# Performance work log

Hardware: AMD Instinct MI355X
Metric: run time of the kernel (lower is better)

## Reference

```python
import jax, jax.numpy as jnp
import numpy as np

NUM_EXPERTS = 64
HIDDEN = 2048
SINKHORN_ITERS = 30
EPS = 1e-08


def setup_inputs() -> dict:
    key = jax.random.key(0)
    k1, k2 = jax.random.split(key)
    hidden_states = jax.random.normal(k1, (4, 2048, HIDDEN), dtype=jnp.float32)
    # torch Linear default init ~ U(-1/sqrt(H), 1/sqrt(H))
    bound = 1.0 / np.sqrt(HIDDEN)
    W = jax.random.uniform(k2, (NUM_EXPERTS, HIDDEN), dtype=jnp.float32,
                           minval=-bound, maxval=bound)
    return {"hidden_states": hidden_states, "W": W}


def _sinkhorn(cost, num_iters=SINKHORN_ITERS):
    # cost: (T, E) float32 logits
    cost = jnp.exp(cost)
    T, E = cost.shape
    d0 = jnp.ones((T,), dtype=cost.dtype)
    d1 = jnp.ones((E,), dtype=cost.dtype)

    def body(i, carry):
        d0, d1 = carry
        d0 = (1.0 / T) / (jnp.sum(d1 * cost, axis=1) + EPS)
        d1 = (1.0 / E) / (jnp.sum(d0[:, None] * cost, axis=0) + EPS)
        return (d0, d1)

    d0, d1 = jax.lax.fori_loop(0, num_iters, body, (d0, d1))
    return d1 * cost * d0[:, None]


def reference(hidden_states, W):
    # router logits: (B, S, H) @ (H, E) -> flatten to (T, E)
    logits = jnp.einsum('bsh,eh->bse', hidden_states, W)
    router_logits = logits.reshape(-1, NUM_EXPERTS)
    # expert affinities (original uses float64 sigmoid; use float32 for jax default)
    expert_affinities = jax.nn.sigmoid(router_logits.astype(jnp.float32))
    expert_affinities = expert_affinities.astype(hidden_states.dtype)
    # Sinkhorn balancing on detached logits (training path)
    sinkroute = _sinkhorn(jax.lax.stop_gradient(router_logits).astype(jnp.float32))
    expert_index = jnp.argmax(sinkroute, axis=1, keepdims=True).astype(jnp.int32)
    return (router_logits, expert_affinities, expert_index)
```

## Files before the change

### kernel.cpp

```cpp
#include <hip/hip_runtime.h>
#include <math.h>

#define T_TOKENS 8192
#define NEXP 64
#define HID 2048
#define NITER 30
#define SINK_BLOCKS 32
#define NCHUNK 32
#define QPC 512
#define WREG 131072

typedef __bf16 bf16_t;
typedef bf16_t bf16x8 __attribute__((ext_vector_type(8)));
typedef bf16_t bf16x4 __attribute__((ext_vector_type(4)));
typedef float  f32x4  __attribute__((ext_vector_type(4)));

__device__ __forceinline__ void gload_lds16(const void* g, void* l) {
    __builtin_amdgcn_global_load_lds(
        (const __attribute__((address_space(1))) unsigned int*)g,
        (__attribute__((address_space(3))) unsigned int*)l, 16, 0, 0);
}

__global__ __launch_bounds__(256)
void prep_whl(const float* __restrict__ W, bf16_t* __restrict__ wsw)
{
    int gid = blockIdx.x * 256 + threadIdx.x;
    int region = gid >> 14;
    int qid = gid & 16383;
    int c = qid >> 9, L = qid & 511;
    int r = L >> 3, slot = L & 7;
    int qi = slot ^ (r & 7);
    const float* src = W + (size_t)r * HID + c * 64 + qi * 8;
    float4 v0 = *(const float4*)src;
    float4 v1 = *(const float4*)(src + 4);
    float x[8] = {v0.x, v0.y, v0.z, v0.w, v1.x, v1.y, v1.z, v1.w};
    bf16x8 q;
#pragma unroll
    for (int i = 0; i < 8; i++) {
        bf16_t h = (bf16_t)x[i];
        q[i] = (region == 0) ? h : (bf16_t)(x[i] - (float)h);
    }
    *(bf16x8*)(wsw + (size_t)region * WREG + (size_t)qid * 8) = q;
}

__global__ __launch_bounds__(256, 2)
void gemm_mfma_split(const float* __restrict__ A, const bf16_t* __restrict__ Wq,
                     float* __restrict__ out)
{
    __shared__ bf16_t sA[2][2][16 * 64];
    __shared__ bf16_t sW[2][2][64 * 64];
    __shared__ float  red[2 * 512];

    const int tid = threadIdx.x, lane = tid & 63, wv = tid >> 6;
    const int tok0 = blockIdx.x * 16;
    const int s = wv >> 1, nh = wv & 1;
    const int g = lane >> 4, m = lane & 15;

    f32x4 acc0 = {0.f, 0.f, 0.f, 0.f}, acc1 = {0.f, 0.f, 0.f, 0.f};

    const int ar = tid >> 4, ak4 = tid & 15;
    const int a_woff = ar * 64 + (((ak4 >> 1) ^ (ar & 7)) << 3) + ((ak4 & 1) << 2);
    const float* ag = A + (size_t)(tok0 + ar) * HID + ak4 * 4;

    const bf16_t* whg = Wq;
    const bf16_t* wlg = Wq + WREG;

    const int aq = s * 4 + g;
    const int a_roff  = m * 64 + ((aq ^ (m & 7)) << 3);
    const int n0 = nh * 32 + m, n1 = n0 + 16;
    const int b_roff0 = n0 * 64 + ((aq ^ (n0 & 7)) << 3);
    const int b_roff1 = n1 * 64 + ((aq ^ (n1 & 7)) << 3);

    {
        float4 av = *(const float4*)ag;
        float xs[4] = {av.x, av.y, av.z, av.w};
        bf16x4 hq, lq;
#pragma unroll
        for (int i = 0; i < 4; i++) {
            bf16_t h = (bf16_t)xs[i];
            hq[i] = h; lq[i] = (bf16_t)(xs[i] - (float)h);
        }
        *(bf16x4*)&sA[0][0][a_woff] = hq;
        *(bf16x4*)&sA[0][1][a_woff] = lq;
#pragma unroll
        for (int j = 0; j < 2; j++) {
            size_t q = (size_t)(j * 256 + wv * 64 + lane) * 8;
            gload_lds16(whg + q, &sW[0][0][(j * 256 + wv * 64) * 8]);
            gload_lds16(wlg + q, &sW[0][1][(j * 256 + wv * 64) * 8]);
        }
    }
    __syncthreads();

    for (int c = 0; c < NCHUNK; ++c) {
        const int buf = c & 1, nb = buf ^ 1;
        if (c + 1 < NCHUNK) {
            const int cn = c + 1;
            float4 av = *(const float4*)(ag + cn * 64);
#pragma unroll
            for (int j = 0; j < 2; j++) {
                size_t q = (size_t)(cn * QPC + j * 256 + wv * 64 + lane) * 8;
                gload_lds16(whg + q, &sW[nb][0][(j * 256 + wv * 64) * 8]);
                gload_lds16(wlg + q, &sW[nb][1][(j * 256 + wv * 64) * 8]);
            }
            float xs[4] = {av.x, av.y, av.z, av.w};
            bf16x4 hq, lq;
#pragma unroll
            for (int i = 0; i < 4; i++) {
                bf16_t h = (bf16_t)xs[i];
                hq[i] = h; lq[i] = (bf16_t)(xs[i] - (float)h);
            }
            *(bf16x4*)&sA[nb][0][a_woff] = hq;
            *(bf16x4*)&sA[nb][1][a_woff] = lq;
        }

        bf16x8 fAh  = *(const bf16x8*)&sA[buf][0][a_roff];
        bf16x8 fAl  = *(const bf16x8*)&sA[buf][1][a_roff];
        bf16x8 fWh0 = *(const bf16x8*)&sW[buf][0][b_roff0];
        bf16x8 fWl0 = *(const bf16x8*)&sW[buf][1][b_roff0];
        bf16x8 fWh1 = *(const bf16x8*)&sW[buf][0][b_roff1];
        bf16x8 fWl1 = *(const bf16x8*)&sW[buf][1][b_roff1];

        acc0 = __builtin_amdgcn_mfma_f32_16x16x32_bf16(fAh, fWh0, acc0, 0, 0, 0);
        acc0 = __builtin_amdgcn_mfma_f32_16x16x32_bf16(fAh, fWl0, acc0, 0, 0, 0);
        acc0 = __builtin_amdgcn_mfma_f32_16x16x32_bf16(fAl, fWh0, acc0, 0, 0, 0);
        acc1 = __builtin_amdgcn_mfma_f32_16x16x32_bf16(fAh, fWh1, acc1, 0, 0, 0);
        acc1 = __builtin_amdgcn_mfma_f32_16x16x32_bf16(fAh, fWl1, acc1, 0, 0, 0);
        acc1 = __builtin_amdgcn_mfma_f32_16x16x32_bf16(fAl, fWh1, acc1, 0, 0, 0);
        __syncthreads();
    }

    if (s == 1) {
#pragma unroll
        for (int i = 0; i < 4; i++) {
            red[nh * 512 + lane * 8 + i]     = acc0[i];
            red[nh * 512 + lane * 8 + 4 + i] = acc1[i];
        }
    }
    __syncthreads();
    if (s == 0) {
        const int t0 = tok0 + (lane >> 4) * 4;
#pragma unroll
        for (int i = 0; i < 4; i++) {
            float v0 = acc0[i] + red[nh * 512 + lane * 8 + i];
            float v1 = acc1[i] + red[nh * 512 + lane * 8 + 4 + i];
            int t = t0 + i;
            out[(size_t)t * 64 + n0] = v0;
            out[(size_t)t * 64 + n1] = v1;
            float s0 = (v0 >= 0.f) ? 1.f / (1.f + expf(-v0))
                                   : expf(v0) / (1.f + expf(v0));
            float s1 = (v1 >= 0.f) ? 1.f / (1.f + expf(-v1))
                                   : expf(v1) / (1.f + expf(v1));
            out[(size_t)T_TOKENS * 64 + (size_t)t * 64 + n0] = s0;
            out[(size_t)T_TOKENS * 64 + (size_t)t * 64 + n1] = s1;
        }
    }
}

__global__ __launch_bounds__(256, 1)
void sinkhorn_v3(const float* __restrict__ logits,
                 float* __restrict__ out_idx,
                 float* __restrict__ part)
{
    __shared__ float tile[4][64 * 68];
    __shared__ float d1_lds[64];
    __shared__ float pl[4][64];
    const int tid = threadIdx.x;
    const int bid = blockIdx.x;
    const int wave = tid >> 6, lane = tid & 63;
    const int t = bid * 256 + tid;

    float c[64];
#pragma unroll
    for (int e4 = 0; e4 < 16; e4++) {
        float4 v = *(const float4*)(logits + (size_t)t * 64 + e4 * 4);
        c[e4 * 4 + 0] = expf(v.x);
        c[e4 * 4 + 1] = expf(v.y);
        c[e4 * 4 + 2] = expf(v.z);
        c[e4 * 4 + 3] = expf(v.w);
    }
    if (tid < 64) d1_lds[tid] = 1.0f;
    __syncthreads();

    float d0 = 0.f;
    float* tw = tile[wave];

    for (int iter = 0; iter < NITER; ++iter) {
        float s = 0.f;
#pragma unroll
        for (int e4 = 0; e4 < 16; e4++) {
            float4 dv = *(const float4*)(&d1_lds[e4 * 4]);
            s = fmaf(c[e4 * 4 + 0], dv.x, s);
            s = fmaf(c[e4 * 4 + 1], dv.y, s);
            s = fmaf(c[e4 * 4 + 2], dv.z, s);
            s = fmaf(c[e4 * 4 + 3], dv.w, s);
        }
        d0 = (1.0f / 8192.0f) / (s + 1e-8f);

#pragma unroll
        for (int e4 = 0; e4 < 16; e4++) {
            float4 v;
            v.x = c[e4 * 4 + 0] * d0; v.y = c[e4 * 4 + 1] * d0;
            v.z = c[e4 * 4 + 2] * d0; v.w = c[e4 * 4 + 3] * d0;
            *(float4*)(&tw[lane * 68 + e4 * 4]) = v;
        }
        __syncthreads();
        float colsum = 0.f;
#pragma unroll 16
        for (int j = 0; j < 64; j++) colsum += tw[j * 68 + lane];
        pl[wave][lane] = colsum;
        __syncthreads();

        if (tid < 64) {
            float S = pl[0][tid] + pl[1][tid] + pl[2][tid] + pl[3][tid];
            __hip_atomic_store(&part[(size_t)(iter * SINK_BLOCKS + bid) * 64 + tid], S,
                               __ATOMIC_RELAXED, __HIP_MEMORY_SCOPE_SYSTEM);
            const float* pb = part + (size_t)iter * SINK_BLOCKS * 64 + tid;
            float v[SINK_BLOCKS];
            bool ok = false; int guard = 0;
            while (!ok && guard++ < (1 << 20)) {
                ok = true;
#pragma unroll
                for (int b = 0; b < SINK_BLOCKS; b++)
                    v[b] = __hip_atomic_load(pb + b * 64, __ATOMIC_RELAXED,
                                             __HIP_MEMORY_SCOPE_SYSTEM);
#pragma unroll
                for (int b = 0; b < SINK_BLOCKS; b++) ok = ok && (v[b] > 0.f);
            }
            float S2 = 0.f;
#pragma unroll
            for (int b = 0; b < SINK_BLOCKS; b++) S2 += v[b];
            d1_lds[tid] = (1.0f / 64.0f) / (S2 + 1e-8f);
        }
        __syncthreads();
    }

    float best = -1.0f; int bi = 0;
#pragma unroll
    for (int e4 = 0; e4 < 16; e4++) {
        float4 dv = *(const float4*)(&d1_lds[e4 * 4]);
        float vv0 = (dv.x * c[e4 * 4 + 0]) * d0;
        float vv1 = (dv.y * c[e4 * 4 + 1]) * d0;
        float vv2 = (dv.z * c[e4 * 4 + 2]) * d0;
        float vv3 = (dv.w * c[e4 * 4 + 3]) * d0;
        if (vv0 > best) { best = vv0; bi = e4 * 4 + 0; }
        if (vv1 > best) { best = vv1; bi = e4 * 4 + 1; }
        if (vv2 > best) { best = vv2; bi = e4 * 4 + 2; }
        if (vv3 > best) { best = vv3; bi = e4 * 4 + 3; }
    }
    out_idx[t] = (float)bi;
}

extern "C" void kernel_launch(void* const* d_in, const int* in_sizes, int n_in,
                              void* d_out, int out_size, void* d_ws, size_t ws_size,
                              hipStream_t stream)
{
    (void)in_sizes; (void)n_in; (void)out_size; (void)ws_size;
    const float* hs = (const float*)d_in[0];
    const float* W  = (const float*)d_in[1];
    float* out      = (float*)d_out;
    bf16_t* wsw     = (bf16_t*)d_ws;
    float* part     = (float*)d_ws + WREG;

    prep_whl<<<128, 256, 0, stream>>>(W, wsw);
    gemm_mfma_split<<<512, 256, 0, stream>>>(hs, wsw, out);
    sinkhorn_v3<<<SINK_BLOCKS, 256, 0, stream>>>(
        out, out + (size_t)2 * T_TOKENS * NEXP, part);
}
```

Baseline: 249.1 us.

## Split-K GEMM with async fp32 A staging and flag-based sinkhorn barrier

Restructures the router GEMM into a two-way split-K over 32-token tiles, staging fp32 activations straight into LDS with async global-to-LDS loads and doing the bf16 hi/lo split at fragment read time. Partial sums go to workspace and the sinkhorn kernel now sums them, writing logits and sigmoid affinities. The inter-block barrier in sinkhorn uses per-block ready flags with agent-scope atomics and sleep instead of polling all partials at system scope. This adds an extra partial buffer round-trip and moves the epilogue onto only 32 blocks.

```diff
diff --git a/kernel.cpp b/kernel.cpp
--- a/kernel.cpp
+++ b/kernel.cpp
@@ -6,13 +6,10 @@
 #define HID 2048
 #define NITER 30
 #define SINK_BLOCKS 32
-#define NCHUNK 32
-#define QPC 512
 #define WREG 131072
 
 typedef __bf16 bf16_t;
 typedef bf16_t bf16x8 __attribute__((ext_vector_type(8)));
-typedef bf16_t bf16x4 __attribute__((ext_vector_type(4)));
 typedef float  f32x4  __attribute__((ext_vector_type(4)));
 
 __device__ __forceinline__ void gload_lds16(const void* g, void* l) {
@@ -44,135 +41,136 @@
 }
 
 __global__ __launch_bounds__(256, 2)
-void gemm_mfma_split(const float* __restrict__ A, const bf16_t* __restrict__ Wq,
-                     float* __restrict__ out)
-{
-    __shared__ bf16_t sA[2][2][16 * 64];
+void gemm_splitk(const float* __restrict__ A, const bf16_t* __restrict__ Wq,
+                 float* __restrict__ part)
+{
+    __shared__ float  sA[2][32 * 64];
     __shared__ bf16_t sW[2][2][64 * 64];
-    __shared__ float  red[2 * 512];
 
     const int tid = threadIdx.x, lane = tid & 63, wv = tid >> 6;
-    const int tok0 = blockIdx.x * 16;
-    const int s = wv >> 1, nh = wv & 1;
+    const int ks   = blockIdx.x & 1;
+    const int tok0 = (blockIdx.x >> 1) * 32;
+    const int mgrp = wv >> 1, ngrp = wv & 1;
     const int g = lane >> 4, m = lane & 15;
+    const int arow = mgrp * 16 + m;
+    const int m7 = m & 7;
 
     f32x4 acc0 = {0.f, 0.f, 0.f, 0.f}, acc1 = {0.f, 0.f, 0.f, 0.f};
 
-    const int ar = tid >> 4, ak4 = tid & 15;
-    const int a_woff = ar * 64 + (((ak4 >> 1) ^ (ar & 7)) << 3) + ((ak4 & 1) << 2);
-    const float* ag = A + (size_t)(tok0 + ar) * HID + ak4 * 4;
-
-    const bf16_t* whg = Wq;
-    const bf16_t* wlg = Wq + WREG;
-
-    const int aq = s * 4 + g;
-    const int a_roff  = m * 64 + ((aq ^ (m & 7)) << 3);
-    const int n0 = nh * 32 + m, n1 = n0 + 16;
-    const int b_roff0 = n0 * 64 + ((aq ^ (n0 & 7)) << 3);
-    const int b_roff1 = n1 * 64 + ((aq ^ (n1 & 7)) << 3);
-
-    {
-        float4 av = *(const float4*)ag;
-        float xs[4] = {av.x, av.y, av.z, av.w};
-        bf16x4 hq, lq;
-#pragma unroll
-        for (int i = 0; i < 4; i++) {
-            bf16_t h = (bf16_t)xs[i];
-            hq[i] = h; lq[i] = (bf16_t)(xs[i] - (float)h);
-        }
-        *(bf16x4*)&sA[0][0][a_woff] = hq;
-        *(bf16x4*)&sA[0][1][a_woff] = lq;
-#pragma unroll
-        for (int j = 0; j < 2; j++) {
-            size_t q = (size_t)(j * 256 + wv * 64 + lane) * 8;
-            gload_lds16(whg + q, &sW[0][0][(j * 256 + wv * 64) * 8]);
-            gload_lds16(wlg + q, &sW[0][1][(j * 256 + wv * 64) * 8]);
-        }
-    }
+    int ap[2], acs[2];
+#pragma unroll
+    for (int j = 0; j < 2; j++) {
+        int p = (wv * 2 + j) * 64 + lane;
+        ap[j] = p;
+        int r = p >> 4, slot = p & 15;
+        acs[j] = slot ^ (r & 7);
+    }
+
+#define STAGE_CHUNK(cc, dst)                                                    \
+    {                                                                           \
+        const int _cc = (cc);                                                   \
+        _Pragma("unroll")                                                       \
+        for (int j = 0; j < 2; j++) {                                           \
+            int r = ap[j] >> 4;                                                 \
+            const float* src = A + (size_t)(tok0 + r) * HID + ks * 1024         \
+                             + _cc * 64 + acs[j] * 4;                           \
+            gload_lds16(src, &sA[dst][(wv * 2 + j) * 256]);                     \
+        }                                                                       \
+        const size_t chb = ((size_t)(ks * 16 + _cc) * 512) * 8;                 \
+        _Pragma("unroll")                                                       \
+        for (int j = 0; j < 2; j++) {                                           \
+            size_t q8 = chb + (size_t)((wv * 2 + j) * 64 + lane) * 8;           \
+            gload_lds16(Wq + q8,        &sW[dst][0][(wv * 2 + j) * 512]);       \
+            gload_lds16(Wq + WREG + q8, &sW[dst][1][(wv * 2 + j) * 512]);       \
+        }                                                                       \
+    }
+
+    STAGE_CHUNK(0, 0);
     __syncthreads();
 
-    for (int c = 0; c < NCHUNK; ++c) {
-        const int buf = c & 1, nb = buf ^ 1;
-        if (c + 1 < NCHUNK) {
-            const int cn = c + 1;
-            float4 av = *(const float4*)(ag + cn * 64);
-#pragma unroll
-            for (int j = 0; j < 2; j++) {
-                size_t q = (size_t)(cn * QPC + j * 256 + wv * 64 + lane) * 8;
-                gload_lds16(whg + q, &sW[nb][0][(j * 256 + wv * 64) * 8]);
-                gload_lds16(wlg + q, &sW[nb][1][(j * 256 + wv * 64) * 8]);
-            }
-            float xs[4] = {av.x, av.y, av.z, av.w};
-            bf16x4 hq, lq;
-#pragma unroll
-            for (int i = 0; i < 4; i++) {
+    for (int cc = 0; cc < 16; ++cc) {
+        const int buf = cc & 1, nb = buf ^ 1;
+        if (cc + 1 < 16) STAGE_CHUNK(cc + 1, nb);
+
+        const float*  sAc = sA[buf];
+        const bf16_t* sWh = sW[buf][0];
+        const bf16_t* sWl = sW[buf][1];
+#pragma unroll
+        for (int k32 = 0; k32 < 2; ++k32) {
+            int s0 = (k32 * 8 + g * 2) ^ m7;
+            float4 x0 = *(const float4*)&sAc[arow * 64 + s0 * 4];
+            float4 x1 = *(const float4*)&sAc[arow * 64 + (s0 ^ 1) * 4];
+            float xs[8] = {x0.x, x0.y, x0.z, x0.w, x1.x, x1.y, x1.z, x1.w};
+            bf16x8 fAh, fAl;
+#pragma unroll
+            for (int i = 0; i < 8; i++) {
                 bf16_t h = (bf16_t)xs[i];
-                hq[i] = h; lq[i] = (bf16_t)(xs[i] - (float)h);
-            }
-            *(bf16x4*)&sA[nb][0][a_woff] = hq;
-            *(bf16x4*)&sA[nb][1][a_woff] = lq;
-        }
-
-        bf16x8 fAh  = *(const bf16x8*)&sA[buf][0][a_roff];
-        bf16x8 fAl  = *(const bf16x8*)&sA[buf][1][a_roff];
-        bf16x8 fWh0 = *(const bf16x8*)&sW[buf][0][b_roff0];
-        bf16x8 fWl0 = *(const bf16x8*)&sW[buf][1][b_roff0];
-        bf16x8 fWh1 = *(const bf16x8*)&sW[buf][0][b_roff1];
-        bf16x8 fWl1 = *(const bf16x8*)&sW[buf][1][b_roff1];
-
-        acc0 = __builtin_amdgcn_mfma_f32_16x16x32_bf16(fAh, fWh0, acc0, 0, 0, 0);
-        acc0 = __builtin_amdgcn_mfma_f32_16x16x32_bf16(fAh, fWl0, acc0, 0, 0, 0);
-        acc0 = __builtin_amdgcn_mfma_f32_16x16x32_bf16(fAl, fWh0, acc0, 0, 0, 0);
-        acc1 = __builtin_amdgcn_mfma_f32_16x16x32_bf16(fAh, fWh1, acc1, 0, 0, 0);
-        acc1 = __builtin_amdgcn_mfma_f32_16x16x32_bf16(fAh, fWl1, acc1, 0, 0, 0);
-        acc1 = __builtin_amdgcn_mfma_f32_16x16x32_bf16(fAl, fWh1, acc1, 0, 0, 0);
-        __syncthreads();
-    }
-
-    if (s == 1) {
-#pragma unroll
-        for (int i = 0; i < 4; i++) {
-            red[nh * 512 + lane * 8 + i]     = acc0[i];
-            red[nh * 512 + lane * 8 + 4 + i] = acc1[i];
-        }
-    }
-    __syncthreads();
-    if (s == 0) {
-        const int t0 = tok0 + (lane >> 4) * 4;
-#pragma unroll
-        for (int i = 0; i < 4; i++) {
-            float v0 = acc0[i] + red[nh * 512 + lane * 8 + i];
-            float v1 = acc1[i] + red[nh * 512 + lane * 8 + 4 + i];
-            int t = t0 + i;
-            out[(size_t)t * 64 + n0] = v0;
-            out[(size_t)t * 64 + n1] = v1;
-            float s0 = (v0 >= 0.f) ? 1.f / (1.f + expf(-v0))
-                                   : expf(v0) / (1.f + expf(v0));
-            float s1 = (v1 >= 0.f) ? 1.f / (1.f + expf(-v1))
-                                   : expf(v1) / (1.f + expf(v1));
-            out[(size_t)T_TOKENS * 64 + (size_t)t * 64 + n0] = s0;
-            out[(size_t)T_TOKENS * 64 + (size_t)t * 64 + n1] = s1;
-        }
-    }
+                fAh[i] = h; fAl[i] = (bf16_t)(xs[i] - (float)h);
+            }
+            const int q = k32 * 4 + g;
+            {
+                int off = (ngrp * 32 + m) * 64 + (q ^ m7) * 8;
+                bf16x8 fWh = *(const bf16x8*)&sWh[off];
+                bf16x8 fWl = *(const bf16x8*)&sWl[off];
+                acc0 = __builtin_amdgcn_mfma_f32_16x16x32_bf16(fAh, fWh, acc0, 0, 0, 0);
+                acc0 = __builtin_amdgcn_mfma_f32_16x16x32_bf16(fAh, fWl, acc0, 0, 0, 0);
+                acc0 = __builtin_amdgcn_mfma_f32_16x16x32_bf16(fAl, fWh, acc0, 0, 0, 0);
+            }
+            {
+                int off = (ngrp * 32 + 16 + m) * 64 + (q ^ m7) * 8;
+                bf16x8 fWh = *(const bf16x8*)&sWh[off];
+                bf16x8 fWl = *(const bf16x8*)&sWl[off];
+                acc1 = __builtin_amdgcn_mfma_f32_16x16x32_bf16(fAh, fWh, acc1, 0, 0, 0);
+                acc1 = __builtin_amdgcn_mfma_f32_16x16x32_bf16(fAh, fWl, acc1, 0, 0, 0);
+                acc1 = __builtin_amdgcn_mfma_f32_16x16x32_bf16(fAl, fWh, acc1, 0, 0, 0);
+            }
+        }
+        __syncthreads();
+    }
+
+    float* pb = part + (size_t)ks * T_TOKENS * 64;
+#pragma unroll
+    for (int i = 0; i < 4; i++) {
+        int t = tok0 + mgrp * 16 + g * 4 + i;
+        pb[(size_t)t * 64 + ngrp * 32 + m]      = acc0[i];
+        pb[(size_t)t * 64 + ngrp * 32 + 16 + m] = acc1[i];
+    }
+#undef STAGE_CHUNK
 }
 
 __global__ __launch_bounds__(256, 1)
-void sinkhorn_v3(const float* __restrict__ logits,
-                 float* __restrict__ out_idx,
-                 float* __restrict__ part)
+void sinkhorn_v4(const float* __restrict__ part,
+                 float* __restrict__ out,
+                 float* __restrict__ sd,
+                 float* __restrict__ fl)
 {
     __shared__ float tile[4][64 * 68];
     __shared__ float d1_lds[64];
     __shared__ float pl[4][64];
-    const int tid = threadIdx.x;
-    const int bid = blockIdx.x;
+    const int tid = threadIdx.x, bid = blockIdx.x;
     const int wave = tid >> 6, lane = tid & 63;
     const int t = bid * 256 + tid;
 
+    float* logits = out;
+    float* aff    = out + (size_t)T_TOKENS * 64;
+    float* idx    = out + (size_t)2 * T_TOKENS * 64;
+
+    const float* p0 = part + (size_t)t * 64;
+    const float* p1 = part + (size_t)T_TOKENS * 64 + (size_t)t * 64;
+
     float c[64];
 #pragma unroll
     for (int e4 = 0; e4 < 16; e4++) {
-        float4 v = *(const float4*)(logits + (size_t)t * 64 + e4 * 4);
+        float4 a = *(const float4*)(p0 + e4 * 4);
+        float4 b = *(const float4*)(p1 + e4 * 4);
+        float4 v = {a.x + b.x, a.y + b.y, a.z + b.z, a.w + b.w};
+        *(float4*)(logits + (size_t)t * 64 + e4 * 4) = v;
+        float4 sg;
+        sg.x = (v.x >= 0.f) ? 1.f / (1.f + expf(-v.x)) : expf(v.x) / (1.f + expf(v.x));
+        sg.y = (v.y >= 0.f) ? 1.f / (1.f + expf(-v.y)) : expf(v.y) / (1.f + expf(v.y));
+        sg.z = (v.z >= 0.f) ? 1.f / (1.f + expf(-v.z)) : expf(v.z) / (1.f + expf(v.z));
+        sg.w = (v.w >= 0.f) ? 1.f / (1.f + expf(-v.w)) : expf(v.w) / (1.f + expf(v.w));
+        *(float4*)(aff + (size_t)t * 64 + e4 * 4) = sg;
         c[e4 * 4 + 0] = expf(v.x);
         c[e4 * 4 + 1] = expf(v.y);
         c[e4 * 4 + 2] = expf(v.z);
@@ -212,20 +210,28 @@
 
         if (tid < 64) {
             float S = pl[0][tid] + pl[1][tid] + pl[2][tid] + pl[3][tid];
-            __hip_atomic_store(&part[(size_t)(iter * SINK_BLOCKS + bid) * 64 + tid], S,
-                               __ATOMIC_RELAXED, __HIP_MEMORY_SCOPE_SYSTEM);
-            const float* pb = part + (size_t)iter * SINK_BLOCKS * 64 + tid;
+            __hip_atomic_store(&sd[(size_t)(iter * SINK_BLOCKS + bid) * 64 + tid], S,
+                               __ATOMIC_RELAXED, __HIP_MEMORY_SCOPE_AGENT);
+            if (tid == 0) {
+                __builtin_amdgcn_fence(__ATOMIC_RELEASE, "agent");
+                __hip_atomic_store(&fl[iter * SINK_BLOCKS + bid], 1.0f,
+                                   __ATOMIC_RELAXED, __HIP_MEMORY_SCOPE_AGENT);
+            }
+            if (tid < SINK_BLOCKS) {
+                int guard = 0;
+                for (;;) {
+                    float f = __hip_atomic_load(&fl[iter * SINK_BLOCKS + tid],
+                                                __ATOMIC_RELAXED, __HIP_MEMORY_SCOPE_AGENT);
+                    if (f > 0.f || ++guard >= (1 << 20)) break;
+                    __builtin_amdgcn_s_sleep(1);
+                }
+            }
+            const float* base = sd + (size_t)iter * SINK_BLOCKS * 64 + tid;
             float v[SINK_BLOCKS];
-            bool ok = false; int guard = 0;
-            while (!ok && guard++ < (1 << 20)) {
-                ok = true;
-#pragma unroll
-                for (int b = 0; b < SINK_BLOCKS; b++)
-                    v[b] = __hip_atomic_load(pb + b * 64, __ATOMIC_RELAXED,
-                                             __HIP_MEMORY_SCOPE_SYSTEM);
-#pragma unroll
-                for (int b = 0; b < SINK_BLOCKS; b++) ok = ok && (v[b] > 0.f);
-            }
+#pragma unroll
+            for (int b = 0; b < SINK_BLOCKS; b++)
+                v[b] = __hip_atomic_load(base + b * 64, __ATOMIC_RELAXED,
+                                         __HIP_MEMORY_SCOPE_AGENT);
             float S2 = 0.f;
 #pragma unroll
             for (int b = 0; b < SINK_BLOCKS; b++) S2 += v[b];
@@ -247,7 +253,7 @@
         if (vv2 > best) { best = vv2; bi = e4 * 4 + 2; }
         if (vv3 > best) { best = vv3; bi = e4 * 4 + 3; }
     }
-    out_idx[t] = (float)bi;
+    idx[t] = (float)bi;
 }
 
 extern "C" void kernel_launch(void* const* d_in, const int* in_sizes, int n_in,
@@ -258,11 +264,13 @@
     const float* hs = (const float*)d_in[0];
     const float* W  = (const float*)d_in[1];
     float* out      = (float*)d_out;
-    bf16_t* wsw     = (bf16_t*)d_ws;
-    float* part     = (float*)d_ws + WREG;
+
+    bf16_t* wsw = (bf16_t*)d_ws;
+    float*  part = (float*)d_ws + 131072;
+    float*  sd   = part + 2 * T_TOKENS * 64;
+    float*  fl   = sd + NITER * SINK_BLOCKS * 64;
 
     prep_whl<<<128, 256, 0, stream>>>(W, wsw);
-    gemm_mfma_split<<<512, 256, 0, stream>>>(hs, wsw, out);
-    sinkhorn_v3<<<SINK_BLOCKS, 256, 0, stream>>>(
-        out, out + (size_t)2 * T_TOKENS * NEXP, part);
-}
+    gemm_splitk<<<512, 256, 0, stream>>>(hs, wsw, part);
+    sinkhorn_v4<<<SINK_BLOCKS, 256, 0, stream>>>(part, out, sd, fl);
+}
```

Measured after the change: 220.3 us. 11.6% less time.
